# Kernel tuning notes

Hardware: AMD Instinct MI355X
Metric: run time of the kernel (lower is better)

Reference implementation:

```python
import jax, jax.numpy as jnp
import numpy as np

N = 200_000      # nodes
DEG = 10         # edges per node (RadiusGraph max_num_neighbors=10, loop=True)
E = N * DEG
F0, F1 = 3, 20   # in features (pos), hidden
EPS = 1e-5       # PyG StdAggregation epsilon


def _glorot(k, shape):
    return jax.random.normal(k, shape, jnp.float32) / jnp.sqrt(jnp.float32(shape[-1]))


def setup_inputs() -> dict:
    key = jax.random.key(0)
    ks = jax.random.split(key, 20)
    x = jax.random.normal(ks[0], (N, F0), jnp.float32)
    # each node gets DEG incoming edges: dst structured, src random; first edge per node is a self-loop
    src = jax.random.randint(ks[1], (E,), 0, N, jnp.int32)
    dst = jnp.repeat(jnp.arange(N, dtype=jnp.int32), DEG)
    src = src.at[::DEG].set(jnp.arange(N, dtype=jnp.int32))  # self-loops
    edge_index = jnp.stack([src, dst])
    return {
        "x": x,
        "edge_index": edge_index,
        # conv1: PNAConv(3, 20)
        "w_pre1": _glorot(ks[2], (F0, 2 * F0)), "b_pre1": jnp.zeros((F0,), jnp.float32),
        "w_post1": _glorot(ks[3], (F1, 17 * F0)), "b_post1": jnp.zeros((F1,), jnp.float32),
        "w_lin1": _glorot(ks[4], (F1, F1)), "b_lin1": jnp.zeros((F1,), jnp.float32),
        # conv2: PNAConv(20, 20)
        "w_pre2": _glorot(ks[5], (F1, 2 * F1)), "b_pre2": jnp.zeros((F1,), jnp.float32),
        "w_post2": _glorot(ks[6], (F1, 17 * F1)), "b_post2": jnp.zeros((F1,), jnp.float32),
        "w_lin2": _glorot(ks[7], (F1, F1)), "b_lin2": jnp.zeros((F1,), jnp.float32),
        # final Linear(20, 1)
        "w_out": _glorot(ks[8], (1, F1)), "b_out": jnp.zeros((1,), jnp.float32),
    }


def _pna(x, src, dst, avg_lin, avg_log, w_pre, b_pre, w_post, b_post, w_lin, b_lin):
    n = x.shape[0]
    # message: pre_nn(x_i || x_j)
    h = jnp.concatenate([x[dst], x[src]], axis=-1)          # [E, 2F]
    m = h @ w_pre.T + b_pre                                 # [E, F]
    cnt = jax.ops.segment_sum(jnp.ones(dst.shape[0], jnp.float32), dst, num_segments=n)
    deg = jnp.maximum(cnt, 1.0)                             # [N]
    s = jax.ops.segment_sum(m, dst, num_segments=n)
    s2 = jax.ops.segment_sum(m * m, dst, num_segments=n)
    mean = s / deg[:, None]
    var = jax.nn.relu(s2 / deg[:, None] - mean * mean)
    std = jnp.sqrt(var + EPS)
    has = (cnt > 0.0)[:, None]
    mn = jnp.where(has, jax.ops.segment_min(m, dst, num_segments=n), 0.0)
    mx = jnp.where(has, jax.ops.segment_max(m, dst, num_segments=n), 0.0)
    agg = jnp.concatenate([mean, mn, mx, std], axis=-1)     # [N, 4F]
    # degree scalers: identity, amplification, attenuation, linear
    logd = jnp.log(deg + 1.0)[:, None]
    out = jnp.concatenate([agg,
                           agg * (logd / avg_log),
                           agg * (avg_log / logd),
                           agg * (deg / avg_lin)[:, None]], axis=-1)  # [N, 16F]
    out = jnp.concatenate([x, out], axis=-1)                # [N, 17F]
    out = out @ w_post.T + b_post                           # post_nn
    return out @ w_lin.T + b_lin                            # final tower mixer


def reference(x, edge_index, w_pre1, b_pre1, w_post1, b_post1, w_lin1, b_lin1,
              w_pre2, b_pre2, w_post2, b_post2, w_lin2, b_lin2, w_out, b_out):
    src, dst = edge_index[0], edge_index[1]
    n = x.shape[0]
    cnt = jax.ops.segment_sum(jnp.ones(dst.shape[0], jnp.float32), dst, num_segments=n)
    avg_lin = cnt.mean()                    # avg_deg['lin'] over the degree histogram
    avg_log = jnp.log(cnt + 1.0).mean()     # avg_deg['log']
    h = jax.nn.relu(_pna(x, src, dst, avg_lin, avg_log, w_pre1, b_pre1, w_post1, b_post1, w_lin1, b_lin1))
    h = jax.nn.relu(_pna(h, src, dst, avg_lin, avg_log, w_pre2, b_pre2, w_post2, b_post2, w_lin2, b_lin2))
    return h @ w_out.T + b_out              # [N, 1]
```

## Files before the change

### kernel.cpp

```cpp
#include <hip/hip_runtime.h>
#include <hip/hip_fp16.h>


#define N_NODES 200000
#define NPB 64
#define NBLK (N_NODES / NPB)
#define FOLD_BLOCKS 196

#define O_WD1  0
#define O_WA1  64
#define O_B1C  304
#define O_WD2  336
#define O_WA2  736
#define O_B2C  2336
#define O_XH   4096
#define O_B2H  404096
#define O_D2H  3604096

__global__ __launch_bounds__(128) void fold_kernel(
    const float* __restrict__ x,
    const float* __restrict__ w_pre1, const float* __restrict__ b_pre1,
    const float* __restrict__ w_post1, const float* __restrict__ b_post1,
    const float* __restrict__ w_lin1,  const float* __restrict__ b_lin1,
    const float* __restrict__ w_pre2, const float* __restrict__ b_pre2,
    const float* __restrict__ w_post2, const float* __restrict__ b_post2,
    const float* __restrict__ w_lin2,  const float* __restrict__ b_lin2,
    float* __restrict__ ws, __half* __restrict__ xh)
{
    __shared__ float wl1[20], wl2[20], c1[51], c2s[340];
    __shared__ float swa1[12], swa2[80], s1[3], s2[20];
    const int j = blockIdx.x;
    const int t = threadIdx.x;

    if (j >= 20) {
        const int stride = (FOLD_BLOCKS - 20) * 128;
        for (int n = (j - 20)*128 + t; n < N_NODES; n += stride) {
            union { __half2 h2[2]; unsigned long long u; } p;
            p.h2[0] = __floats2half2_rn(x[n*3+0], x[n*3+1]);
            p.h2[1] = __floats2half2_rn(x[n*3+2], 0.f);
            *(unsigned long long*)&xh[n*4] = p.u;
        }
        return;
    }

    if (t < 20) { wl1[t] = w_lin1[j*20 + t]; wl2[t] = w_lin2[j*20 + t]; }
    __syncthreads();
    for (int c = t; c < 51; c += 128) {
        float a = 0.f;
        #pragma unroll
        for (int k = 0; k < 20; ++k) a += wl1[k] * w_post1[k*51 + c];
        c1[c] = a;
    }
    for (int c = t; c < 340; c += 128) {
        float a = 0.f;
        #pragma unroll
        for (int k = 0; k < 20; ++k) a += wl2[k] * w_post2[k*340 + c];
        c2s[c] = a;
    }
    __syncthreads();
    if (t < 12) swa1[t] = c1[3+t]  + c1[15+t]  + c1[27+t]  + c1[39+t];
    if (t < 80) swa2[t] = c2s[20+t] + c2s[100+t] + c2s[180+t] + c2s[260+t];
    __syncthreads();
    if (t < 3)  s1[t] = swa1[t] + swa1[3+t]  + swa1[6+t];
    if (t < 20) s2[t] = swa2[t] + swa2[20+t] + swa2[40+t];
    if (t < 12) ws[O_WA1 + j*12 + t] = swa1[t];
    if (t < 80) ws[O_WA2 + j*80 + t] = swa2[t];
    __syncthreads();
    if (t < 3) {
        float a = c1[t];
        #pragma unroll
        for (int r = 0; r < 3; ++r) a += s1[r] * w_pre1[r*6 + t];
        ws[O_WD1 + j*3 + t] = a;
    }
    if (t < 20) {
        float a = c2s[t];
        #pragma unroll
        for (int r = 0; r < 20; ++r) a += s2[r] * w_pre2[r*40 + t];
        ws[O_WD2 + j*20 + t] = a;
    }
    if (t == 0) {
        float a = b_lin1[j];
        #pragma unroll
        for (int k = 0; k < 20; ++k) a += wl1[k] * b_post1[k];
        #pragma unroll
        for (int r = 0; r < 3;  ++r) a += s1[r] * b_pre1[r];
        ws[O_B1C + j] = a;
        float b = b_lin2[j];
        #pragma unroll
        for (int k = 0; k < 20; ++k) b += wl2[k] * b_post2[k];
        #pragma unroll
        for (int r = 0; r < 20; ++r) b += s2[r] * b_pre2[r];
        ws[O_B2C + j] = b;
    }
}

__global__ __launch_bounds__(320) void k1_kernel(
    const __half* __restrict__ xh, const int* __restrict__ src,
    const float* __restrict__ w_pre1, const float* __restrict__ w_pre2,
    const float* __restrict__ ws,
    __half* __restrict__ b2h, __half* __restrict__ d2h)
{
    __shared__ float sAgg[NPB * 13];
    __shared__ float sH1[NPB * 21];
    const int t = threadIdx.x;
    const int node0 = blockIdx.x * NPB;

    const int pil = t & 63;
    union { unsigned long long u; __half2 h2[2]; } pxi;
    pxi.u = *(const unsigned long long*)&xh[(node0 + pil)*4];

    if (t < 192) {
        const int il = t / 3, f = t - (t/3)*3;
        const float w3 = w_pre1[f*6+3], w4 = w_pre1[f*6+4], w5 = w_pre1[f*6+5];
        union { unsigned long long u; __half2 h2[2]; } v;
        v.u = *(const unsigned long long*)&xh[(node0 + il)*4];
        float2 ab = __half22float2(v.h2[0]);
        float2 cd = __half22float2(v.h2[1]);
        const float m0 = w3*ab.x + w4*ab.y + w5*cd.x;
        float sum = m0, sq = m0*m0, mn = m0, mx = m0;
        #pragma unroll
        for (int e = 1; e < 10; ++e) {
            const int sj = src[node0*10 + il*10 + e];
            v.u = *(const unsigned long long*)&xh[sj*4];
            ab = __half22float2(v.h2[0]);
            cd = __half22float2(v.h2[1]);
            const float m = w3*ab.x + w4*ab.y + w5*cd.x;
            sum += m; sq += m*m; mn = fminf(mn, m); mx = fmaxf(mx, m);
        }
        const float mean = sum * 0.1f;
        const float var  = fmaxf(sq * 0.1f - mean*mean, 0.f);
        sAgg[il*13 + 0 + f] = mean;
        sAgg[il*13 + 3 + f] = mn;
        sAgg[il*13 + 6 + f] = mx;
        sAgg[il*13 + 9 + f] = sqrtf(var + 1e-5f);
    }
    __syncthreads();

    const int wv = __builtin_amdgcn_readfirstlane(t >> 6);
    const int il = t & 63;
    const int node = node0 + il;
    const int f0 = wv * 4;

    const float2 xab = __half22float2(pxi.h2[0]);
    const float2 xcd = __half22float2(pxi.h2[1]);
    const float xi0 = xab.x, xi1 = xab.y, xi2 = xcd.x;

    float ag[12];
    #pragma unroll
    for (int k = 0; k < 12; ++k) ag[k] = sAgg[il*13 + k];
    #pragma unroll
    for (int ff = 0; ff < 4; ++ff) {
        const int f = f0 + ff;
        float acc = ws[O_B1C + f]
            + ws[O_WD1 + f*3+0]*xi0 + ws[O_WD1 + f*3+1]*xi1 + ws[O_WD1 + f*3+2]*xi2;
        #pragma unroll
        for (int k = 0; k < 12; ++k) acc += ws[O_WA1 + f*12 + k] * ag[k];
        sH1[il*21 + f] = fmaxf(acc, 0.f);
    }
    __syncthreads();

    float hk[20];
    #pragma unroll
    for (int k = 0; k < 20; ++k) hk[k] = sH1[il*21 + k];
    float vb[4], vd[4];
    #pragma unroll
    for (int ff = 0; ff < 4; ++ff) {
        const int f = f0 + ff;
        float B = 0.f, D = ws[O_B2C + f];
        #pragma unroll
        for (int k = 0; k < 20; ++k) {
            B += w_pre2[f*40 + 20 + k] * hk[k];
            D += ws[O_WD2 + f*20 + k]  * hk[k];
        }
        vb[ff] = B; vd[ff] = D;
    }
    union { __half2 h2[2]; unsigned long long u; } pb, pd;
    pb.h2[0] = __floats2half2_rn(vb[0], vb[1]);
    pb.h2[1] = __floats2half2_rn(vb[2], vb[3]);
    pd.h2[0] = __floats2half2_rn(vd[0], vd[1]);
    pd.h2[1] = __floats2half2_rn(vd[2], vd[3]);
    *(unsigned long long*)&b2h[node*32 + f0] = pb.u;
    *(unsigned long long*)&d2h[node*20 + f0] = pd.u;
}

__global__ __launch_bounds__(320) void k2_kernel(
    const int* __restrict__ src, const float* __restrict__ ws,
    const __half* __restrict__ b2h, const __half* __restrict__ d2h,
    const float* __restrict__ w_out, const float* __restrict__ b_out,
    float* __restrict__ out)
{
    __shared__ float sAgg[NPB * 81];
    __shared__ float sPart[320];
    const int t = threadIdx.x;
    const int node0 = blockIdx.x * NPB;

    const int pil = t & 63;
    const int pf0 = (t >> 6) * 4;
    union { unsigned long long u; __half2 h2[2]; } pdd;
    pdd.u = *(const unsigned long long*)&d2h[(node0+pil)*20 + pf0];

    {
        const int il = t / 5, fq = t - (t/5)*5;
        const int f0 = fq * 4;
        int sj[10];
        sj[0] = node0 + il;
        #pragma unroll
        for (int e = 1; e < 10; ++e) sj[e] = src[node0*10 + il*10 + e];
        float s[4]  = {0.f, 0.f, 0.f, 0.f};
        float q[4]  = {0.f, 0.f, 0.f, 0.f};
        float mn[4] = {1e30f, 1e30f, 1e30f, 1e30f};
        float mx[4] = {-1e30f, -1e30f, -1e30f, -1e30f};
        #pragma unroll
        for (int e = 0; e < 10; ++e) {
            union { uint2 u; __half2 h2[2]; } v;
            v.u = *(const uint2*)&b2h[sj[e]*32 + f0];
            const float2 a = __half22float2(v.h2[0]);
            const float2 b = __half22float2(v.h2[1]);
            const float fv[4] = {a.x, a.y, b.x, b.y};
            #pragma unroll
            for (int j = 0; j < 4; ++j) {
                s[j] += fv[j]; q[j] += fv[j]*fv[j];
                mn[j] = fminf(mn[j], fv[j]); mx[j] = fmaxf(mx[j], fv[j]);
            }
        }
        #pragma unroll
        for (int j = 0; j < 4; ++j) {
            const int f = f0 + j;
            const float me = s[j] * 0.1f;
            const float sd = sqrtf(fmaxf(q[j]*0.1f - me*me, 0.f) + 1e-5f);
            sAgg[il*81 + f]      = me;
            sAgg[il*81 + 20 + f] = mn[j];
            sAgg[il*81 + 40 + f] = mx[j];
            sAgg[il*81 + 60 + f] = sd;
        }
    }
    __syncthreads();

    const int wv = __builtin_amdgcn_readfirstlane(t >> 6);
    const int il = t & 63;
    const int f0 = wv * 4;

    const float2 d01 = __half22float2(pdd.h2[0]);
    const float2 d23 = __half22float2(pdd.h2[1]);
    float acc0 = d01.x, acc1 = d01.y, acc2 = d23.x, acc3 = d23.y;
    #pragma unroll
    for (int k = 0; k < 80; ++k) {
        const float ag = sAgg[il*81 + k];
        acc0 += ws[O_WA2 + (f0+0)*80 + k] * ag;
        acc1 += ws[O_WA2 + (f0+1)*80 + k] * ag;
        acc2 += ws[O_WA2 + (f0+2)*80 + k] * ag;
        acc3 += ws[O_WA2 + (f0+3)*80 + k] * ag;
    }
    const float py = w_out[f0+0]*fmaxf(acc0, 0.f) + w_out[f0+1]*fmaxf(acc1, 0.f)
                   + w_out[f0+2]*fmaxf(acc2, 0.f) + w_out[f0+3]*fmaxf(acc3, 0.f);
    sPart[wv*64 + il] = py;
    __syncthreads();

    if (t < 64) {
        float y = b_out[0];
        #pragma unroll
        for (int v = 0; v < 5; ++v) y += sPart[v*64 + t];
        out[node0 + t] = y;
    }
}

extern "C" void kernel_launch(void* const* d_in, const int* in_sizes, int n_in,
                              void* d_out, int out_size, void* d_ws, size_t ws_size,
                              hipStream_t stream)
{
    const float* x       = (const float*)d_in[0];
    const int*   eidx    = (const int*)  d_in[1];
    const float* w_pre1  = (const float*)d_in[2];
    const float* b_pre1  = (const float*)d_in[3];
    const float* w_post1 = (const float*)d_in[4];
    const float* b_post1 = (const float*)d_in[5];
    const float* w_lin1  = (const float*)d_in[6];
    const float* b_lin1  = (const float*)d_in[7];
    const float* w_pre2  = (const float*)d_in[8];
    const float* b_pre2  = (const float*)d_in[9];
    const float* w_post2 = (const float*)d_in[10];
    const float* b_post2 = (const float*)d_in[11];
    const float* w_lin2  = (const float*)d_in[12];
    const float* b_lin2  = (const float*)d_in[13];
    const float* w_out   = (const float*)d_in[14];
    const float* b_out   = (const float*)d_in[15];
    float* out = (float*)d_out;
    float* ws  = (float*)d_ws;
    __half* xh  = (__half*)(ws + O_XH);
    __half* b2h = (__half*)(ws + O_B2H);
    __half* d2h = (__half*)(ws + O_D2H);

    fold_kernel<<<FOLD_BLOCKS, 128, 0, stream>>>(x,
                                        w_pre1, b_pre1, w_post1, b_post1,
                                        w_lin1, b_lin1, w_pre2, b_pre2,
                                        w_post2, b_post2, w_lin2, b_lin2,
                                        ws, xh);
    k1_kernel<<<NBLK, 320, 0, stream>>>(xh, eidx, w_pre1, w_pre2, ws, b2h, d2h);
    k2_kernel<<<NBLK, 320, 0, stream>>>(eidx, ws, b2h, d2h, w_out, b_out, out);
}
```

Before: 62.69 us.

## Fuse fold, layer-1 and layer-2 kernels into one cooperative persistent kernel

Merges the three kernel launches into a single cooperative kernel that uses grid-wide syncs between the weight-fold/half-conversion phase, the layer-1 aggregation and the layer-2 aggregation. Blocks loop persistently over node groups, and the shared memory of the three phases is overlaid through a union. The aim is to remove launch gaps between kernels. In exchange, occupancy is capped at co-resident blocks, grid.sync adds its own overhead, and host-side attribute and occupancy queries now run on every call.

Result: slower. 243.0 us (+287.6%).

```diff
diff --git a/kernel.cpp b/kernel.cpp
--- a/kernel.cpp
+++ b/kernel.cpp
@@ -1,5 +1,8 @@
 #include <hip/hip_runtime.h>
 #include <hip/hip_fp16.h>
+#include <hip/hip_cooperative_groups.h>
+
+namespace cg = cooperative_groups;
 
 
 #define N_NODES 200000
@@ -17,41 +20,27 @@
 #define O_B2H  404096
 #define O_D2H  3604096
 
-__global__ __launch_bounds__(128) void fold_kernel(
-    const float* __restrict__ x,
+__device__ __forceinline__ void fold_body(
+    int j, int t, int nthreads,
     const float* __restrict__ w_pre1, const float* __restrict__ b_pre1,
     const float* __restrict__ w_post1, const float* __restrict__ b_post1,
     const float* __restrict__ w_lin1,  const float* __restrict__ b_lin1,
     const float* __restrict__ w_pre2, const float* __restrict__ b_pre2,
     const float* __restrict__ w_post2, const float* __restrict__ b_post2,
     const float* __restrict__ w_lin2,  const float* __restrict__ b_lin2,
-    float* __restrict__ ws, __half* __restrict__ xh)
-{
-    __shared__ float wl1[20], wl2[20], c1[51], c2s[340];
-    __shared__ float swa1[12], swa2[80], s1[3], s2[20];
-    const int j = blockIdx.x;
-    const int t = threadIdx.x;
-
-    if (j >= 20) {
-        const int stride = (FOLD_BLOCKS - 20) * 128;
-        for (int n = (j - 20)*128 + t; n < N_NODES; n += stride) {
-            union { __half2 h2[2]; unsigned long long u; } p;
-            p.h2[0] = __floats2half2_rn(x[n*3+0], x[n*3+1]);
-            p.h2[1] = __floats2half2_rn(x[n*3+2], 0.f);
-            *(unsigned long long*)&xh[n*4] = p.u;
-        }
-        return;
-    }
-
+    float* __restrict__ ws,
+    float* wl1, float* wl2, float* c1, float* c2s,
+    float* swa1, float* swa2, float* s1, float* s2)
+{
     if (t < 20) { wl1[t] = w_lin1[j*20 + t]; wl2[t] = w_lin2[j*20 + t]; }
     __syncthreads();
-    for (int c = t; c < 51; c += 128) {
+    for (int c = t; c < 51; c += nthreads) {
         float a = 0.f;
         #pragma unroll
         for (int k = 0; k < 20; ++k) a += wl1[k] * w_post1[k*51 + c];
         c1[c] = a;
     }
-    for (int c = t; c < 340; c += 128) {
+    for (int c = t; c < 340; c += nthreads) {
         float a = 0.f;
         #pragma unroll
         for (int k = 0; k < 20; ++k) a += wl2[k] * w_post2[k*340 + c];
@@ -94,36 +83,33 @@
     }
 }
 
-__global__ __launch_bounds__(320) void k1_kernel(
+__device__ __forceinline__ void l1_body(
+    int node0, int t,
     const __half* __restrict__ xh, const int* __restrict__ src,
     const float* __restrict__ w_pre1, const float* __restrict__ w_pre2,
     const float* __restrict__ ws,
-    __half* __restrict__ b2h, __half* __restrict__ d2h)
-{
-    __shared__ float sAgg[NPB * 13];
-    __shared__ float sH1[NPB * 21];
-    const int t = threadIdx.x;
-    const int node0 = blockIdx.x * NPB;
-
+    __half* __restrict__ b2h, __half* __restrict__ d2h,
+    float* sAgg , float* sH1 )
+{
     const int pil = t & 63;
-    union { unsigned long long u; __half2 h2[2]; } pxi;
-    pxi.u = *(const unsigned long long*)&xh[(node0 + pil)*4];
+    union { unsigned long long v; __half2 h2[2]; } pxi;
+    pxi.v = *(const unsigned long long*)&xh[(node0 + pil)*4];
 
     if (t < 192) {
         const int il = t / 3, f = t - (t/3)*3;
         const float w3 = w_pre1[f*6+3], w4 = w_pre1[f*6+4], w5 = w_pre1[f*6+5];
-        union { unsigned long long u; __half2 h2[2]; } v;
-        v.u = *(const unsigned long long*)&xh[(node0 + il)*4];
-        float2 ab = __half22float2(v.h2[0]);
-        float2 cd = __half22float2(v.h2[1]);
+        union { unsigned long long v; __half2 h2[2]; } vv;
+        vv.v = *(const unsigned long long*)&xh[(node0 + il)*4];
+        float2 ab = __half22float2(vv.h2[0]);
+        float2 cd = __half22float2(vv.h2[1]);
         const float m0 = w3*ab.x + w4*ab.y + w5*cd.x;
         float sum = m0, sq = m0*m0, mn = m0, mx = m0;
         #pragma unroll
         for (int e = 1; e < 10; ++e) {
             const int sj = src[node0*10 + il*10 + e];
-            v.u = *(const unsigned long long*)&xh[sj*4];
-            ab = __half22float2(v.h2[0]);
-            cd = __half22float2(v.h2[1]);
+            vv.v = *(const unsigned long long*)&xh[sj*4];
+            ab = __half22float2(vv.h2[0]);
+            cd = __half22float2(vv.h2[1]);
             const float m = w3*ab.x + w4*ab.y + w5*cd.x;
             sum += m; sq += m*m; mn = fminf(mn, m); mx = fmaxf(mx, m);
         }
@@ -174,30 +160,27 @@
         }
         vb[ff] = B; vd[ff] = D;
     }
-    union { __half2 h2[2]; unsigned long long u; } pb, pd;
+    union { __half2 h2[2]; unsigned long long v; } pb, pd;
     pb.h2[0] = __floats2half2_rn(vb[0], vb[1]);
     pb.h2[1] = __floats2half2_rn(vb[2], vb[3]);
     pd.h2[0] = __floats2half2_rn(vd[0], vd[1]);
     pd.h2[1] = __floats2half2_rn(vd[2], vd[3]);
-    *(unsigned long long*)&b2h[node*32 + f0] = pb.u;
-    *(unsigned long long*)&d2h[node*20 + f0] = pd.u;
-}
-
-__global__ __launch_bounds__(320) void k2_kernel(
+    *(unsigned long long*)&b2h[node*32 + f0] = pb.v;
+    *(unsigned long long*)&d2h[node*20 + f0] = pd.v;
+}
+
+__device__ __forceinline__ void l2_body(
+    int node0, int t,
     const int* __restrict__ src, const float* __restrict__ ws,
     const __half* __restrict__ b2h, const __half* __restrict__ d2h,
     const float* __restrict__ w_out, const float* __restrict__ b_out,
-    float* __restrict__ out)
-{
-    __shared__ float sAgg[NPB * 81];
-    __shared__ float sPart[320];
-    const int t = threadIdx.x;
-    const int node0 = blockIdx.x * NPB;
-
+    float* __restrict__ out,
+    float* sAgg , float* sPart )
+{
     const int pil = t & 63;
     const int pf0 = (t >> 6) * 4;
-    union { unsigned long long u; __half2 h2[2]; } pdd;
-    pdd.u = *(const unsigned long long*)&d2h[(node0+pil)*20 + pf0];
+    union { unsigned long long v; __half2 h2[2]; } pdd;
+    pdd.v = *(const unsigned long long*)&d2h[(node0+pil)*20 + pf0];
 
     {
         const int il = t / 5, fq = t - (t/5)*5;
@@ -212,8 +195,8 @@
         float mx[4] = {-1e30f, -1e30f, -1e30f, -1e30f};
         #pragma unroll
         for (int e = 0; e < 10; ++e) {
-            union { uint2 u; __half2 h2[2]; } v;
-            v.u = *(const uint2*)&b2h[sj[e]*32 + f0];
+            union { uint2 uu; __half2 h2[2]; } v;
+            v.uu = *(const uint2*)&b2h[sj[e]*32 + f0];
             const float2 a = __half22float2(v.h2[0]);
             const float2 b = __half22float2(v.h2[1]);
             const float fv[4] = {a.x, a.y, b.x, b.y};
@@ -262,6 +245,116 @@
         for (int v = 0; v < 5; ++v) y += sPart[v*64 + t];
         out[node0 + t] = y;
     }
+}
+
+__global__ __launch_bounds__(320) void mega_kernel(
+    const float* __restrict__ x, const int* __restrict__ src,
+    const float* __restrict__ w_pre1, const float* __restrict__ b_pre1,
+    const float* __restrict__ w_post1, const float* __restrict__ b_post1,
+    const float* __restrict__ w_lin1,  const float* __restrict__ b_lin1,
+    const float* __restrict__ w_pre2, const float* __restrict__ b_pre2,
+    const float* __restrict__ w_post2, const float* __restrict__ b_post2,
+    const float* __restrict__ w_lin2,  const float* __restrict__ b_lin2,
+    const float* __restrict__ w_out,   const float* __restrict__ b_out,
+    float* __restrict__ ws, float* __restrict__ out)
+{
+    __half* xh  = (__half*)(ws + O_XH);
+    __half* b2h = (__half*)(ws + O_B2H);
+    __half* d2h = (__half*)(ws + O_D2H);
+
+    cg::grid_group grid = cg::this_grid();
+    const int t = threadIdx.x;
+    const int bid = blockIdx.x;
+    const int nb  = gridDim.x;
+
+    __shared__ union SU {
+        struct { float wl1[20], wl2[20], c1[51], c2s[340],
+                       swa1[12], swa2[80], s1[3], s2[20]; } f;
+        struct { float sAgg[NPB*13], sH1[NPB*21]; } a;
+        struct { float sAgg[NPB*81], sPart[320]; } b;
+    } u;
+
+    if (bid < 20) {
+        fold_body(bid, t, 320, w_pre1, b_pre1, w_post1, b_post1, w_lin1, b_lin1,
+                  w_pre2, b_pre2, w_post2, b_post2, w_lin2, b_lin2, ws,
+                  u.f.wl1, u.f.wl2, u.f.c1, u.f.c2s, u.f.swa1, u.f.swa2,
+                  u.f.s1, u.f.s2);
+    } else {
+        const int stride = (nb - 20) * 320;
+        for (int n = (bid - 20)*320 + t; n < N_NODES; n += stride) {
+            union { __half2 h2[2]; unsigned long long v; } p;
+            p.h2[0] = __floats2half2_rn(x[n*3+0], x[n*3+1]);
+            p.h2[1] = __floats2half2_rn(x[n*3+2], 0.f);
+            *(unsigned long long*)&xh[n*4] = p.v;
+        }
+    }
+    grid.sync();
+
+    for (int g = bid; g < NBLK; g += nb) {
+        l1_body(g*NPB, t, xh, src, w_pre1, w_pre2, ws, b2h, d2h,
+                u.a.sAgg, u.a.sH1);
+        __syncthreads();
+    }
+    grid.sync();
+
+    for (int g = bid; g < NBLK; g += nb) {
+        l2_body(g*NPB, t, src, ws, b2h, d2h, w_out, b_out, out,
+                u.b.sAgg, u.b.sPart);
+        __syncthreads();
+    }
+}
+
+__global__ __launch_bounds__(128) void fold_kernel(
+    const float* __restrict__ x,
+    const float* __restrict__ w_pre1, const float* __restrict__ b_pre1,
+    const float* __restrict__ w_post1, const float* __restrict__ b_post1,
+    const float* __restrict__ w_lin1,  const float* __restrict__ b_lin1,
+    const float* __restrict__ w_pre2, const float* __restrict__ b_pre2,
+    const float* __restrict__ w_post2, const float* __restrict__ b_post2,
+    const float* __restrict__ w_lin2,  const float* __restrict__ b_lin2,
+    float* __restrict__ ws, __half* __restrict__ xh)
+{
+    __shared__ float wl1[20], wl2[20], c1[51], c2s[340];
+    __shared__ float swa1[12], swa2[80], s1[3], s2[20];
+    const int j = blockIdx.x;
+    const int t = threadIdx.x;
+    if (j >= 20) {
+        const int stride = (FOLD_BLOCKS - 20) * 128;
+        for (int n = (j - 20)*128 + t; n < N_NODES; n += stride) {
+            union { __half2 h2[2]; unsigned long long v; } p;
+            p.h2[0] = __floats2half2_rn(x[n*3+0], x[n*3+1]);
+            p.h2[1] = __floats2half2_rn(x[n*3+2], 0.f);
+            *(unsigned long long*)&xh[n*4] = p.v;
+        }
+        return;
+    }
+    fold_body(j, t, 128, w_pre1, b_pre1, w_post1, b_post1, w_lin1, b_lin1,
+              w_pre2, b_pre2, w_post2, b_post2, w_lin2, b_lin2, ws,
+              wl1, wl2, c1, c2s, swa1, swa2, s1, s2);
+}
+
+__global__ __launch_bounds__(320) void k1_kernel(
+    const __half* __restrict__ xh, const int* __restrict__ src,
+    const float* __restrict__ w_pre1, const float* __restrict__ w_pre2,
+    const float* __restrict__ ws,
+    __half* __restrict__ b2h, __half* __restrict__ d2h)
+{
+    __shared__ float sAgg[NPB * 13];
+    __shared__ float sH1[NPB * 21];
+    l1_body(blockIdx.x*NPB, threadIdx.x, xh, src, w_pre1, w_pre2, ws,
+            b2h, d2h, sAgg, sH1);
+}
+
+__global__ __launch_bounds__(320) void k2_kernel(
+    const int* __restrict__ src, const float* __restrict__ ws,
+    const __half* __restrict__ b2h, const __half* __restrict__ d2h,
+    const float* __restrict__ w_out, const float* __restrict__ b_out,
+    float* __restrict__ out)
+{
+    __shared__ float sAgg[NPB * 81];
+    __shared__ float sPart[320];
+    l2_body(blockIdx.x*NPB, threadIdx.x, src, ws, b2h, d2h, w_out, b_out,
+            out, sAgg, sPart);
 }
 
 extern "C" void kernel_launch(void* const* d_in, const int* in_sizes, int n_in,
@@ -290,11 +383,38 @@
     __half* b2h = (__half*)(ws + O_B2H);
     __half* d2h = (__half*)(ws + O_D2H);
 
-    fold_kernel<<<FOLD_BLOCKS, 128, 0, stream>>>(x,
-                                        w_pre1, b_pre1, w_post1, b_post1,
-                                        w_lin1, b_lin1, w_pre2, b_pre2,
-                                        w_post2, b_post2, w_lin2, b_lin2,
-                                        ws, xh);
-    k1_kernel<<<NBLK, 320, 0, stream>>>(xh, eidx, w_pre1, w_pre2, ws, b2h, d2h);
-    k2_kernel<<<NBLK, 320, 0, stream>>>(eidx, ws, b2h, d2h, w_out, b_out, out);
-}
+    bool launched = false;
+    int coopOK = 0, numCU = 0, maxB = 0;
+    int dev = 0;
+    (void)hipGetDevice(&dev);
+    (void)hipDeviceGetAttribute(&coopOK, hipDeviceAttributeCooperativeLaunch, dev);
+    (void)hipDeviceGetAttribute(&numCU, hipDeviceAttributeMultiprocessorCount, dev);
+    (void)hipOccupancyMaxActiveBlocksPerMultiprocessor(&maxB, mega_kernel, 320, 0);
+    if (coopOK && numCU > 0 && maxB > 0) {
+        int grid = maxB * numCU;
+        if (grid > NBLK) grid = NBLK;
+        if (grid >= 64) {
+            void* args[] = {
+                (void*)&x, (void*)&eidx,
+                (void*)&w_pre1, (void*)&b_pre1, (void*)&w_post1, (void*)&b_post1,
+                (void*)&w_lin1, (void*)&b_lin1, (void*)&w_pre2, (void*)&b_pre2,
+                (void*)&w_post2, (void*)&b_post2, (void*)&w_lin2, (void*)&b_lin2,
+                (void*)&w_out, (void*)&b_out, (void*)&ws, (void*)&out
+            };
+            hipError_t e = hipLaunchCooperativeKernel((const void*)mega_kernel,
+                                                      dim3(grid), dim3(320),
+                                                      (void**)args, 0, stream);
+            launched = (e == hipSuccess);
+        }
+    }
+    if (!launched) {
+        (void)hipGetLastError();
+        fold_kernel<<<FOLD_BLOCKS, 128, 0, stream>>>(x,
+                                            w_pre1, b_pre1, w_post1, b_post1,
+                                            w_lin1, b_lin1, w_pre2, b_pre2,
+                                            w_post2, b_post2, w_lin2, b_lin2,
+                                            ws, xh);
+        k1_kernel<<<NBLK, 320, 0, stream>>>(xh, eidx, w_pre1, w_pre2, ws, b2h, d2h);
+        k2_kernel<<<NBLK, 320, 0, stream>>>(eidx, ws, b2h, d2h, w_out, b_out, out);
+    }
+}
```

## Use one thread per node in k2 with quarter-split gather layout

Applied to the files above, without the earlier changes.

k1 now writes the layer-2 message features as five separate planes of 4 halves each, instead of one padded 32-half row per node. k2 is rewritten so each thread handles one node. It gathers neighbor features plane by plane, computes the aggregates in registers, and multiplies them by a transposed weight copy (added in the fold kernel) with no shared memory or block syncs. This removes the shared-memory staging and the 32-half padding, so gather traffic is smaller. The cost is heavy register pressure (20 accumulators plus 9 indices) and uncoalesced per-thread weight reads, which should be uniform broadcasts.

Result: slower. 88.59 us (+41.3%).

```diff
diff --git a/kernel.cpp b/kernel.cpp
--- a/kernel.cpp
+++ b/kernel.cpp
@@ -5,17 +5,19 @@
 #define N_NODES 200000
 #define NPB 64
 #define NBLK (N_NODES / NPB)
+#define K2BLK (N_NODES / 320)
 #define FOLD_BLOCKS 196
 
-#define O_WD1  0
-#define O_WA1  64
-#define O_B1C  304
-#define O_WD2  336
-#define O_WA2  736
-#define O_B2C  2336
-#define O_XH   4096
-#define O_B2H  404096
-#define O_D2H  3604096
+#define O_WD1   0
+#define O_WA1   64
+#define O_B1C   304
+#define O_WD2   336
+#define O_WA2   736
+#define O_B2C   2336
+#define O_WA2T  2400
+#define O_XH    4096
+#define O_BQ    404096
+#define O_D2H   2404096
 
 __global__ __launch_bounds__(128) void fold_kernel(
     const float* __restrict__ x,
@@ -35,10 +37,10 @@
     if (j >= 20) {
         const int stride = (FOLD_BLOCKS - 20) * 128;
         for (int n = (j - 20)*128 + t; n < N_NODES; n += stride) {
-            union { __half2 h2[2]; unsigned long long u; } p;
+            union { __half2 h2[2]; unsigned long long v; } p;
             p.h2[0] = __floats2half2_rn(x[n*3+0], x[n*3+1]);
             p.h2[1] = __floats2half2_rn(x[n*3+2], 0.f);
-            *(unsigned long long*)&xh[n*4] = p.u;
+            *(unsigned long long*)&xh[n*4] = p.v;
         }
         return;
     }
@@ -65,6 +67,7 @@
     if (t < 20) s2[t] = swa2[t] + swa2[20+t] + swa2[40+t];
     if (t < 12) ws[O_WA1 + j*12 + t] = swa1[t];
     if (t < 80) ws[O_WA2 + j*80 + t] = swa2[t];
+    if (t < 80) ws[O_WA2T + t*20 + j] = swa2[t];
     __syncthreads();
     if (t < 3) {
         float a = c1[t];
@@ -98,7 +101,7 @@
     const __half* __restrict__ xh, const int* __restrict__ src,
     const float* __restrict__ w_pre1, const float* __restrict__ w_pre2,
     const float* __restrict__ ws,
-    __half* __restrict__ b2h, __half* __restrict__ d2h)
+    __half* __restrict__ bqh, __half* __restrict__ d2h)
 {
     __shared__ float sAgg[NPB * 13];
     __shared__ float sH1[NPB * 21];
@@ -106,24 +109,24 @@
     const int node0 = blockIdx.x * NPB;
 
     const int pil = t & 63;
-    union { unsigned long long u; __half2 h2[2]; } pxi;
-    pxi.u = *(const unsigned long long*)&xh[(node0 + pil)*4];
+    union { unsigned long long v; __half2 h2[2]; } pxi;
+    pxi.v = *(const unsigned long long*)&xh[(node0 + pil)*4];
 
     if (t < 192) {
         const int il = t / 3, f = t - (t/3)*3;
         const float w3 = w_pre1[f*6+3], w4 = w_pre1[f*6+4], w5 = w_pre1[f*6+5];
-        union { unsigned long long u; __half2 h2[2]; } v;
-        v.u = *(const unsigned long long*)&xh[(node0 + il)*4];
-        float2 ab = __half22float2(v.h2[0]);
-        float2 cd = __half22float2(v.h2[1]);
+        union { unsigned long long v; __half2 h2[2]; } vv;
+        vv.v = *(const unsigned long long*)&xh[(node0 + il)*4];
+        float2 ab = __half22float2(vv.h2[0]);
+        float2 cd = __half22float2(vv.h2[1]);
         const float m0 = w3*ab.x + w4*ab.y + w5*cd.x;
         float sum = m0, sq = m0*m0, mn = m0, mx = m0;
         #pragma unroll
         for (int e = 1; e < 10; ++e) {
             const int sj = src[node0*10 + il*10 + e];
-            v.u = *(const unsigned long long*)&xh[sj*4];
-            ab = __half22float2(v.h2[0]);
-            cd = __half22float2(v.h2[1]);
+            vv.v = *(const unsigned long long*)&xh[sj*4];
+            ab = __half22float2(vv.h2[0]);
+            cd = __half22float2(vv.h2[1]);
             const float m = w3*ab.x + w4*ab.y + w5*cd.x;
             sum += m; sq += m*m; mn = fminf(mn, m); mx = fmaxf(mx, m);
         }
@@ -174,94 +177,89 @@
         }
         vb[ff] = B; vd[ff] = D;
     }
-    union { __half2 h2[2]; unsigned long long u; } pb, pd;
+    union { __half2 h2[2]; unsigned long long v; } pb, pd;
     pb.h2[0] = __floats2half2_rn(vb[0], vb[1]);
     pb.h2[1] = __floats2half2_rn(vb[2], vb[3]);
     pd.h2[0] = __floats2half2_rn(vd[0], vd[1]);
     pd.h2[1] = __floats2half2_rn(vd[2], vd[3]);
-    *(unsigned long long*)&b2h[node*32 + f0] = pb.u;
-    *(unsigned long long*)&d2h[node*20 + f0] = pd.u;
+    *(unsigned long long*)&bqh[((size_t)wv*N_NODES + node)*4] = pb.v;
+    *(unsigned long long*)&d2h[(size_t)node*20 + f0] = pd.v;
 }
 
 __global__ __launch_bounds__(320) void k2_kernel(
     const int* __restrict__ src, const float* __restrict__ ws,
-    const __half* __restrict__ b2h, const __half* __restrict__ d2h,
+    const __half* __restrict__ bqh, const __half* __restrict__ d2h,
     const float* __restrict__ w_out, const float* __restrict__ b_out,
     float* __restrict__ out)
 {
-    __shared__ float sAgg[NPB * 81];
-    __shared__ float sPart[320];
     const int t = threadIdx.x;
-    const int node0 = blockIdx.x * NPB;
-
-    const int pil = t & 63;
-    const int pf0 = (t >> 6) * 4;
-    union { unsigned long long u; __half2 h2[2]; } pdd;
-    pdd.u = *(const unsigned long long*)&d2h[(node0+pil)*20 + pf0];
-
-    {
-        const int il = t / 5, fq = t - (t/5)*5;
-        const int f0 = fq * 4;
-        int sj[10];
-        sj[0] = node0 + il;
-        #pragma unroll
-        for (int e = 1; e < 10; ++e) sj[e] = src[node0*10 + il*10 + e];
-        float s[4]  = {0.f, 0.f, 0.f, 0.f};
-        float q[4]  = {0.f, 0.f, 0.f, 0.f};
-        float mn[4] = {1e30f, 1e30f, 1e30f, 1e30f};
-        float mx[4] = {-1e30f, -1e30f, -1e30f, -1e30f};
-        #pragma unroll
-        for (int e = 0; e < 10; ++e) {
-            union { uint2 u; __half2 h2[2]; } v;
-            v.u = *(const uint2*)&b2h[sj[e]*32 + f0];
-            const float2 a = __half22float2(v.h2[0]);
-            const float2 b = __half22float2(v.h2[1]);
-            const float fv[4] = {a.x, a.y, b.x, b.y};
+    const int node = blockIdx.x * 320 + t;
+
+    int sj[9];
+    #pragma unroll
+    for (int e = 0; e < 9; ++e) sj[e] = src[node*10 + 1 + e];
+
+    float acc[20];
+    #pragma unroll
+    for (int f = 0; f < 20; ++f) acc[f] = 0.f;
+
+    #pragma unroll
+    for (int q = 0; q < 5; ++q) {
+        const __half* tq = bqh + (size_t)q * N_NODES * 4;
+        union { unsigned long long v; __half2 h2[2]; } g;
+        g.v = *(const unsigned long long*)&tq[(size_t)node*4];
+        float2 p0 = __half22float2(g.h2[0]);
+        float2 p1 = __half22float2(g.h2[1]);
+        float sm[4] = {p0.x, p0.y, p1.x, p1.y};
+        float sq[4] = {p0.x*p0.x, p0.y*p0.y, p1.x*p1.x, p1.y*p1.y};
+        float mn[4] = {p0.x, p0.y, p1.x, p1.y};
+        float mx[4] = {p0.x, p0.y, p1.x, p1.y};
+        #pragma unroll
+        for (int e = 0; e < 9; ++e) {
+            g.v = *(const unsigned long long*)&tq[(size_t)sj[e]*4];
+            p0 = __half22float2(g.h2[0]);
+            p1 = __half22float2(g.h2[1]);
+            const float fv[4] = {p0.x, p0.y, p1.x, p1.y};
             #pragma unroll
             for (int j = 0; j < 4; ++j) {
-                s[j] += fv[j]; q[j] += fv[j]*fv[j];
+                sm[j] += fv[j]; sq[j] += fv[j]*fv[j];
                 mn[j] = fminf(mn[j], fv[j]); mx[j] = fmaxf(mx[j], fv[j]);
             }
         }
+        float st[16];
         #pragma unroll
         for (int j = 0; j < 4; ++j) {
-            const int f = f0 + j;
-            const float me = s[j] * 0.1f;
-            const float sd = sqrtf(fmaxf(q[j]*0.1f - me*me, 0.f) + 1e-5f);
-            sAgg[il*81 + f]      = me;
-            sAgg[il*81 + 20 + f] = mn[j];
-            sAgg[il*81 + 40 + f] = mx[j];
-            sAgg[il*81 + 60 + f] = sd;
-        }
-    }
-    __syncthreads();
-
-    const int wv = __builtin_amdgcn_readfirstlane(t >> 6);
-    const int il = t & 63;
-    const int f0 = wv * 4;
-
-    const float2 d01 = __half22float2(pdd.h2[0]);
-    const float2 d23 = __half22float2(pdd.h2[1]);
-    float acc0 = d01.x, acc1 = d01.y, acc2 = d23.x, acc3 = d23.y;
-    #pragma unroll
-    for (int k = 0; k < 80; ++k) {
-        const float ag = sAgg[il*81 + k];
-        acc0 += ws[O_WA2 + (f0+0)*80 + k] * ag;
-        acc1 += ws[O_WA2 + (f0+1)*80 + k] * ag;
-        acc2 += ws[O_WA2 + (f0+2)*80 + k] * ag;
-        acc3 += ws[O_WA2 + (f0+3)*80 + k] * ag;
-    }
-    const float py = w_out[f0+0]*fmaxf(acc0, 0.f) + w_out[f0+1]*fmaxf(acc1, 0.f)
-                   + w_out[f0+2]*fmaxf(acc2, 0.f) + w_out[f0+3]*fmaxf(acc3, 0.f);
-    sPart[wv*64 + il] = py;
-    __syncthreads();
-
-    if (t < 64) {
-        float y = b_out[0];
-        #pragma unroll
-        for (int v = 0; v < 5; ++v) y += sPart[v*64 + t];
-        out[node0 + t] = y;
-    }
+            const float me = sm[j] * 0.1f;
+            st[j]      = me;
+            st[4 + j]  = mn[j];
+            st[8 + j]  = mx[j];
+            st[12 + j] = sqrtf(fmaxf(sq[j]*0.1f - me*me, 0.f) + 1e-5f);
+        }
+        #pragma unroll
+        for (int b = 0; b < 4; ++b) {
+            #pragma unroll
+            for (int j = 0; j < 4; ++j) {
+                const float v = st[b*4 + j];
+                const float* wrow = &ws[O_WA2T + (b*20 + q*4 + j)*20];
+                #pragma unroll
+                for (int f = 0; f < 20; ++f) acc[f] += wrow[f] * v;
+            }
+        }
+    }
+
+    float y = b_out[0];
+    #pragma unroll
+    for (int p = 0; p < 5; ++p) {
+        union { unsigned long long v; __half2 h2[2]; } dd;
+        dd.v = *(const unsigned long long*)&d2h[(size_t)node*20 + p*4];
+        const float2 a = __half22float2(dd.h2[0]);
+        const float2 b = __half22float2(dd.h2[1]);
+        y += w_out[p*4+0]*fmaxf(acc[p*4+0] + a.x, 0.f)
+           + w_out[p*4+1]*fmaxf(acc[p*4+1] + a.y, 0.f)
+           + w_out[p*4+2]*fmaxf(acc[p*4+2] + b.x, 0.f)
+           + w_out[p*4+3]*fmaxf(acc[p*4+3] + b.y, 0.f);
+    }
+    out[node] = y;
 }
 
 extern "C" void kernel_launch(void* const* d_in, const int* in_sizes, int n_in,
@@ -287,7 +285,7 @@
     float* out = (float*)d_out;
     float* ws  = (float*)d_ws;
     __half* xh  = (__half*)(ws + O_XH);
-    __half* b2h = (__half*)(ws + O_B2H);
+    __half* bqh = (__half*)(ws + O_BQ);
     __half* d2h = (__half*)(ws + O_D2H);
 
     fold_kernel<<<FOLD_BLOCKS, 128, 0, stream>>>(x,
@@ -295,6 +293,6 @@
                                         w_lin1, b_lin1, w_pre2, b_pre2,
                                         w_post2, b_post2, w_lin2, b_lin2,
                                         ws, xh);
-    k1_kernel<<<NBLK, 320, 0, stream>>>(xh, eidx, w_pre1, w_pre2, ws, b2h, d2h);
-    k2_kernel<<<NBLK, 320, 0, stream>>>(eidx, ws, b2h, d2h, w_out, b_out, out);
-}
+    k1_kernel<<<NBLK, 320, 0, stream>>>(xh, eidx, w_pre1, w_pre2, ws, bqh, d2h);
+    k2_kernel<<<K2BLK, 320, 0, stream>>>(eidx, ws, bqh, d2h, w_out, b_out, out);
+}
```
